# Kernel tuning notes

Measured on AMD Instinct MI355X. Metric: run time of the kernel, lower is better.

Reference implementation:

```python
import jax, jax.numpy as jnp
import numpy as np

D_IN = 512
D = 1024      # new_embed_dim
H = 16        # num_heads
HD = D // H   # head_dim


def setup_inputs() -> dict:
    key = jax.random.key(0)
    ks = jax.random.split(key, 16)
    g = lambda k, shape, fan: jax.random.normal(k, shape, jnp.float32) / np.sqrt(fan)
    return {
        "x1": jax.random.normal(ks[0], (16, 1, D_IN), jnp.float32),
        "x2": jax.random.normal(ks[1], (16, 4096, D_IN), jnp.float32),
        "x3": jax.random.normal(ks[2], (16, 4096, D_IN), jnp.float32),
        # embedding1 (for x1) and embedding2 (used for BOTH x2 and x3, per source)
        "We1": g(ks[3], (D_IN, D), D_IN), "be1": jnp.zeros((D,), jnp.float32),
        "We2": g(ks[4], (D_IN, D), D_IN), "be2": jnp.zeros((D,), jnp.float32),
        "Wq": g(ks[5], (D, D), D), "bq": jnp.zeros((D,), jnp.float32),
        "Wk": g(ks[6], (D, D), D), "bk": jnp.zeros((D,), jnp.float32),
        "Wv": g(ks[7], (D, D), D), "bv": jnp.zeros((D,), jnp.float32),
        "Wo": g(ks[8], (D, D), D), "bo": jnp.zeros((D,), jnp.float32),
    }


def reference(x1, x2, x3, We1, be1, We2, be2, Wq, bq, Wk, bk, Wv, bv, Wo, bo):
    B = x1.shape[0]
    # embeddings (x3 intentionally uses embedding2's weights, matching source)
    x1e = x1 @ We1 + be1                      # [B,1,D]
    x2e = x2 @ We2 + be2                      # [B,S,D]
    x3e = x3 @ We2 + be2                      # [B,S,D]
    q = (x1e @ Wq + bq).reshape(B, -1, H, HD).transpose(0, 2, 1, 3)  # [B,H,1,HD]
    k = (x2e @ Wk + bk).reshape(B, -1, H, HD).transpose(0, 2, 1, 3)  # [B,H,S,HD]
    v = (x3e @ Wv + bv).reshape(B, -1, H, HD).transpose(0, 2, 1, 3)  # [B,H,S,HD]
    scale = jnp.asarray(np.sqrt(HD), q.dtype)
    attn = jax.nn.softmax(jnp.einsum("bhqd,bhkd->bhqk", q, k) / scale, axis=-1)
    # dropout is identity at inference (keras training=False default)
    av = jnp.einsum("bhqk,bhkd->bhqd", attn, v)          # [B,H,1,HD]
    av = av.transpose(0, 2, 1, 3).reshape(B, -1, D)      # [B,1,D]
    out = av @ Wo + bo                                   # [B,1,D]
    return jnp.squeeze(out, axis=1)                      # [B,D]
```

## Files before the change

kernel.cpp:

```cpp
#include <hip/hip_runtime.h>


#define DIN 512
#define DD  1024
#define NH  16
#define HD  64
#define BB  16
#define SS  4096
#define NCH 64

__device__ __forceinline__ int wave_id() {
    return __builtin_amdgcn_readfirstlane((int)(threadIdx.x >> 6));
}

__device__ __forceinline__ void tile_transpose(const float* __restrict__ in,
                                               float* __restrict__ out,
                                               int R, int C, int rblk, int cblk) {
    __shared__ float tl[32][33];
    const int tx = threadIdx.x & 31, ty = threadIdx.x >> 5;
    const int c0 = cblk * 32, r0 = rblk * 32;
#pragma unroll
    for (int k = 0; k < 4; ++k)
        tl[ty + k * 8][tx] = in[(size_t)(r0 + ty + k * 8) * C + c0 + tx];
    __syncthreads();
#pragma unroll
    for (int k = 0; k < 4; ++k)
        out[(size_t)(c0 + ty + k * 8) * R + r0 + tx] = tl[tx][ty + k * 8];
}

__global__ __launch_bounds__(256) void k_prep(const float* __restrict__ We2,
                                              const float* __restrict__ Wk,
                                              const float* __restrict__ be1,
                                              const float* __restrict__ bq,
                                              const float* __restrict__ bv,
                                              const float* __restrict__ bo,
                                              float* __restrict__ We2t,
                                              float* __restrict__ WkT,
                                              float* __restrict__ x1e,
                                              float* __restrict__ qb,
                                              float* __restrict__ av,
                                              float* __restrict__ out) {
    const int bx = blockIdx.x;
    if (bx < 512) {
        tile_transpose(We2, We2t, DIN, DD, bx >> 5, bx & 31);
    } else if (bx < 1536) {
        const int lb = bx - 512;
        tile_transpose(Wk, WkT, DD, DD, lb >> 5, lb & 31);
    } else {
        const int b = bx - 1536;
#pragma unroll
        for (int k = 0; k < 4; ++k) {
            const int c = k * 256 + threadIdx.x;
            x1e[(size_t)b * DD + c] = be1[c];
            qb[(size_t)b * DD + c]  = bq[c];
            av[(size_t)b * DD + c]  = bv[c];
            out[(size_t)b * DD + c] = bo[c];
        }
    }
}

template <int K, int N, int KS, bool HASB>
__global__ __launch_bounds__(256) void k_bmv2(const float* __restrict__ in,
                                              const float* __restrict__ W,
                                              const float* __restrict__ bias,
                                              float* __restrict__ out) {
    const int l = threadIdx.x & 63;
    const int c = blockIdx.x * 64 + l;
    const int wv = wave_id();
    constexpr int KCH = K / KS;
    constexpr int SUB = KCH / 4;
    const float* inb = in + (size_t)blockIdx.y * 16 * K;
    float acc[16];
#pragma unroll
    for (int r = 0; r < 16; ++r) acc[r] = 0.f;
    const int i0 = blockIdx.z * KCH + wv * SUB;
#pragma unroll 4
    for (int i = i0; i < i0 + SUB; ++i) {
        const float wval = W[(size_t)i * N + c];
#pragma unroll
        for (int r = 0; r < 16; ++r) acc[r] += inb[(size_t)r * K + i] * wval;
    }
    __shared__ float red[4][16][64];
#pragma unroll
    for (int r = 0; r < 16; ++r) red[wv][r][l] = acc[r];
    __syncthreads();
#pragma unroll
    for (int k = 0; k < 4; ++k) {
        const int r = wv + k * 4;
        float v = red[0][r][l] + red[1][r][l] + red[2][r][l] + red[3][r][l];
        float* dst = out + ((size_t)blockIdx.y * 16 + r) * N + c;
        if (KS == 1) {
            if (HASB) v += bias[c];
            *dst = v;
        } else {
            atomicAdd(dst, v);
        }
    }
}

__global__ __launch_bounds__(256) void k_u2(const float* __restrict__ q,
                                            const float* __restrict__ WkT,
                                            float* __restrict__ u) {
    const int h = blockIdx.y;
    const int l = threadIdx.x & 63;
    const int c = blockIdx.x * 64 + l;
    const int wv = wave_id();
    float acc[16];
#pragma unroll
    for (int bb = 0; bb < 16; ++bb) acc[bb] = 0.f;
#pragma unroll 4
    for (int dk = 0; dk < 16; ++dk) {
        const int d = wv * 16 + dk;
        const float wval = WkT[(size_t)(h * HD + d) * DD + c];
#pragma unroll
        for (int bb = 0; bb < 16; ++bb)
            acc[bb] += q[(size_t)bb * DD + h * HD + d] * wval;
    }
    __shared__ float red[4][16][64];
#pragma unroll
    for (int bb = 0; bb < 16; ++bb) red[wv][bb][l] = acc[bb];
    __syncthreads();
#pragma unroll
    for (int k = 0; k < 4; ++k) {
        const int bb = wv + k * 4;
        float v = red[0][bb][l] + red[1][bb][l] + red[2][bb][l] + red[3][bb][l];
        u[((size_t)bb * NH + h) * DD + c] = v;
    }
}

__global__ __launch_bounds__(512, 8) void k_attn(const float* __restrict__ x2,
                                                 const float* __restrict__ x3,
                                                 const float* __restrict__ w,
                                                 float* __restrict__ gp,
                                                 float* __restrict__ mls) {
    __shared__ __align__(16) float4 tile[64 * 33];
    __shared__ __align__(16) float etab[64 * 20];

    const int b = blockIdx.y, ch = blockIdx.x;
    const int l = threadIdx.x & 63;
    const int wv = wave_id();
    const int h0 = wv * 2;
    const int s0 = ch * 64;
    const float4* wp = (const float4*)(w + ((size_t)b * NH + h0) * DIN);
    const float4* x2f = (const float4*)x2 + ((size_t)b * SS + s0) * (DIN / 4);

    float a0 = 0.f, a1 = 0.f;
    for (int kt = 0; kt < 4; ++kt) {
#pragma unroll
        for (int k = 0; k < 4; ++k) {
            const int idx = threadIdx.x + k * 512;
            const int row = idx >> 5, c4 = idx & 31;
            tile[row * 33 + c4] = x2f[(size_t)row * 128 + kt * 32 + c4];
        }
        __syncthreads();
#pragma unroll 8
        for (int c4 = 0; c4 < 32; ++c4) {
            const float4 x = tile[l * 33 + c4];
            const float4 q0 = wp[kt * 32 + c4];
            const float4 q1 = wp[128 + kt * 32 + c4];
            a0 += x.x * q0.x + x.y * q0.y + x.z * q0.z + x.w * q0.w;
            a1 += x.x * q1.x + x.y * q1.y + x.z * q1.z + x.w * q1.w;
        }
        __syncthreads();
    }

    const float sc0 = a0 * 0.125f, sc1 = a1 * 0.125f;
    float m0 = sc0, m1 = sc1;
#pragma unroll
    for (int off = 1; off < 64; off <<= 1) {
        m0 = fmaxf(m0, __shfl_xor(m0, off));
        m1 = fmaxf(m1, __shfl_xor(m1, off));
    }
    const float e0 = __expf(sc0 - m0), e1 = __expf(sc1 - m1);
    etab[l * 20 + h0]     = e0;
    etab[l * 20 + h0 + 1] = e1;
    float ls0 = e0, ls1 = e1;
#pragma unroll
    for (int off = 1; off < 64; off <<= 1) {
        ls0 += __shfl_xor(ls0, off);
        ls1 += __shfl_xor(ls1, off);
    }
    if (l == 0) {
        float* dst = mls + (((size_t)b * NCH + ch) * NH + h0) * 2;
        dst[0] = m0; dst[1] = ls0;
        dst[2] = m1; dst[3] = ls1;
    }
    __syncthreads();

    const int col = wv * 64 + l;
    const float* x3c = x3 + ((size_t)b * SS + s0) * DIN + col;
    float acc[16];
#pragma unroll
    for (int h = 0; h < 16; ++h) acc[h] = 0.f;

    float x0 = x3c[0];
    float x1 = x3c[DIN];
    float x2r = x3c[2 * DIN];
    float x3r = x3c[3 * DIN];
#pragma unroll 4
    for (int j = 0; j < 64; ++j) {
        const float xv = x0;
        x0 = x1; x1 = x2r; x2r = x3r;
        const int jn = (j + 4 < 64) ? (j + 4) : 63;
        x3r = x3c[(size_t)jn * DIN];
        const float4 ea = *(const float4*)&etab[j * 20];
        const float4 eb = *(const float4*)&etab[j * 20 + 4];
        const float4 ec = *(const float4*)&etab[j * 20 + 8];
        const float4 ed = *(const float4*)&etab[j * 20 + 12];
        acc[0]  += ea.x * xv;  acc[1]  += ea.y * xv;
        acc[2]  += ea.z * xv;  acc[3]  += ea.w * xv;
        acc[4]  += eb.x * xv;  acc[5]  += eb.y * xv;
        acc[6]  += eb.z * xv;  acc[7]  += eb.w * xv;
        acc[8]  += ec.x * xv;  acc[9]  += ec.y * xv;
        acc[10] += ec.z * xv;  acc[11] += ec.w * xv;
        acc[12] += ed.x * xv;  acc[13] += ed.y * xv;
        acc[14] += ed.z * xv;  acc[15] += ed.w * xv;
    }

    float* gb = gp + ((size_t)(b * NCH + ch) * NH) * DIN + col;
#pragma unroll
    for (int h = 0; h < 16; ++h)
        gb[(size_t)h * DIN] = acc[h];
}

__global__ __launch_bounds__(256) void k_greduce2(const float* __restrict__ gp,
                                                  const float* __restrict__ mls,
                                                  float* __restrict__ g) {
    const int bx = blockIdx.x;
    const int pair = bx >> 1;
    const int b = pair >> 4, h = pair & 15;
    const int i = (bx & 1) * 256 + threadIdx.x;
    const float* mbase = mls + ((size_t)b * NCH * NH + h) * 2;
    float M = -1e30f;
#pragma unroll 8
    for (int ch = 0; ch < NCH; ++ch)
        M = fmaxf(M, mbase[(size_t)ch * NH * 2]);
    float L = 0.f;
#pragma unroll 8
    for (int ch = 0; ch < NCH; ++ch)
        L += __expf(mbase[(size_t)ch * NH * 2] - M) * mbase[(size_t)ch * NH * 2 + 1];
    const float invL = 1.f / L;
    const float* gpb = gp + ((size_t)(b * NCH) * NH + h) * DIN + i;
    float acc = 0.f;
#pragma unroll 8
    for (int ch = 0; ch < NCH; ++ch)
        acc += __expf(mbase[(size_t)ch * NH * 2] - M) * gpb[(size_t)ch * NH * DIN];
    g[(size_t)pair * DIN + i] = acc * invL;
}

__global__ __launch_bounds__(256) void k_av_at(const float* __restrict__ G2,
                                               const float* __restrict__ Wv,
                                               float* __restrict__ av) {
    const int h = blockIdx.x;
    const int l = threadIdx.x & 63;
    const int wv = wave_id();
    const int c0 = blockIdx.y * 128 + wv * 32;
    float acc[16];
#pragma unroll
    for (int bb = 0; bb < 16; ++bb) acc[bb] = 0.f;
#pragma unroll 4
    for (int c = c0; c < c0 + 32; ++c) {
        const float wval = Wv[(size_t)c * DD + h * HD + l];
#pragma unroll
        for (int bb = 0; bb < 16; ++bb)
            acc[bb] += G2[((size_t)bb * NH + h) * DD + c] * wval;
    }
    __shared__ float red[4][16][64];
#pragma unroll
    for (int bb = 0; bb < 16; ++bb) red[wv][bb][l] = acc[bb];
    __syncthreads();
#pragma unroll
    for (int k = 0; k < 4; ++k) {
        const int bb = wv + k * 4;
        float v = red[0][bb][l] + red[1][bb][l] + red[2][bb][l] + red[3][bb][l];
        atomicAdd(&av[(size_t)bb * DD + h * HD + l], v);
    }
}

extern "C" void kernel_launch(void* const* d_in, const int* in_sizes, int n_in,
                              void* d_out, int out_size, void* d_ws, size_t ws_size,
                              hipStream_t stream) {
    const float* x1  = (const float*)d_in[0];
    const float* x2  = (const float*)d_in[1];
    const float* x3  = (const float*)d_in[2];
    const float* We1 = (const float*)d_in[3];
    const float* be1 = (const float*)d_in[4];
    const float* We2 = (const float*)d_in[5];
    const float* be2 = (const float*)d_in[6];
    const float* Wq  = (const float*)d_in[7];
    const float* bq  = (const float*)d_in[8];
    const float* Wk  = (const float*)d_in[9];
    const float* bk  = (const float*)d_in[10];
    const float* Wv  = (const float*)d_in[11];
    const float* bv  = (const float*)d_in[12];
    const float* Wo  = (const float*)d_in[13];
    const float* bo  = (const float*)d_in[14];
    (void)bk;
    float* out = (float*)d_out;

    char* ws = (char*)d_ws;
    size_t off = 0;
    auto alloc = [&](size_t bytes) -> void* {
        void* p = ws + off;
        off = (off + bytes + 255) & ~(size_t)255;
        return p;
    };
    float* We2t = (float*)alloc((size_t)DD * DIN * 4);
    float* WkT  = (float*)alloc((size_t)DD * DD * 4);
    float* x1e  = (float*)alloc((size_t)BB * DD * 4);
    float* qb   = (float*)alloc((size_t)BB * DD * 4);
    float* u    = (float*)alloc((size_t)BB * NH * DD * 4);
    float* wv_  = (float*)alloc((size_t)BB * NH * DIN * 4);
    float* g    = (float*)alloc((size_t)BB * NH * DIN * 4);
    float* G2   = (float*)alloc((size_t)BB * NH * DD * 4);
    float* av   = (float*)alloc((size_t)BB * DD * 4);
    float* gp   = (float*)alloc((size_t)BB * NCH * NH * DIN * 4);
    float* mls  = (float*)alloc((size_t)BB * NCH * NH * 2 * 4);

    k_prep<<<1552, 256, 0, stream>>>(We2, Wk, be1, bq, bv, bo,
                                     We2t, WkT, x1e, qb, av, out);
    k_bmv2<DIN, DD, 8, false><<<dim3(DD / 64, 1, 8), 256, 0, stream>>>(x1, We1, nullptr, x1e);
    k_bmv2<DD, DD, 8, false><<<dim3(DD / 64, 1, 8), 256, 0, stream>>>(x1e, Wq, nullptr, qb);
    k_u2<<<dim3(DD / 64, NH), 256, 0, stream>>>(qb, WkT, u);
    k_bmv2<DD, DIN, 1, false><<<dim3(DIN / 64, BB * NH / 16, 1), 256, 0, stream>>>(u, We2t, nullptr, wv_);
    k_attn<<<dim3(NCH, BB), 512, 0, stream>>>(x2, x3, wv_, gp, mls);
    k_greduce2<<<BB * NH * 2, 256, 0, stream>>>(gp, mls, g);
    k_bmv2<DIN, DD, 1, true><<<dim3(DD / 64, BB * NH / 16, 1), 256, 0, stream>>>(g, We2, be2, G2);
    k_av_at<<<dim3(NH, 8), 256, 0, stream>>>(G2, Wv, av);
    k_bmv2<DD, DD, 8, false><<<dim3(DD / 64, 1, 8), 256, 0, stream>>>(av, Wo, nullptr, out);
}
```

Measured before the change: 446.9 us.

## Prefetch x2 tiles into registers and vectorize x3 weighted-sum loads

The score phase of the attention kernel now loads the next x2 tile into registers while the current tile is being consumed from shared memory. This overlaps global-load latency with compute and drops one barrier per iteration. The value phase is remapped so each wave handles 4 heads across 4 contiguous columns and uses float4 loads and stores for x3 and the partial outputs. This replaces scalar 16-head accumulation, cutting load instruction count and LDS reads at the cost of more live registers.

```diff
diff --git a/kernel.cpp b/kernel.cpp
--- a/kernel.cpp
+++ b/kernel.cpp
@@ -144,15 +144,27 @@
     const float4* wp = (const float4*)(w + ((size_t)b * NH + h0) * DIN);
     const float4* x2f = (const float4*)x2 + ((size_t)b * SS + s0) * (DIN / 4);
 
+    const int srow = threadIdx.x >> 5;
+    const int sc4  = threadIdx.x & 31;
+    float4 r0 = x2f[(size_t)(srow)      * 128 + sc4];
+    float4 r1 = x2f[(size_t)(srow + 16) * 128 + sc4];
+    float4 r2 = x2f[(size_t)(srow + 32) * 128 + sc4];
+    float4 r3 = x2f[(size_t)(srow + 48) * 128 + sc4];
     float a0 = 0.f, a1 = 0.f;
     for (int kt = 0; kt < 4; ++kt) {
-#pragma unroll
-        for (int k = 0; k < 4; ++k) {
-            const int idx = threadIdx.x + k * 512;
-            const int row = idx >> 5, c4 = idx & 31;
-            tile[row * 33 + c4] = x2f[(size_t)row * 128 + kt * 32 + c4];
+        __syncthreads();
+        tile[(srow)      * 33 + sc4] = r0;
+        tile[(srow + 16) * 33 + sc4] = r1;
+        tile[(srow + 32) * 33 + sc4] = r2;
+        tile[(srow + 48) * 33 + sc4] = r3;
+        __syncthreads();
+        if (kt < 3) {
+            const int kc = (kt + 1) * 32 + sc4;
+            r0 = x2f[(size_t)(srow)      * 128 + kc];
+            r1 = x2f[(size_t)(srow + 16) * 128 + kc];
+            r2 = x2f[(size_t)(srow + 32) * 128 + kc];
+            r3 = x2f[(size_t)(srow + 48) * 128 + kc];
         }
-        __syncthreads();
 #pragma unroll 8
         for (int c4 = 0; c4 < 32; ++c4) {
             const float4 x = tile[l * 33 + c4];
@@ -161,7 +173,6 @@
             a0 += x.x * q0.x + x.y * q0.y + x.z * q0.z + x.w * q0.w;
             a1 += x.x * q1.x + x.y * q1.y + x.z * q1.z + x.w * q1.w;
         }
-        __syncthreads();
     }
 
     const float sc0 = a0 * 0.125f, sc1 = a1 * 0.125f;
@@ -187,40 +198,35 @@
     }
     __syncthreads();
 
-    const int col = wv * 64 + l;
-    const float* x3c = x3 + ((size_t)b * SS + s0) * DIN + col;
-    float acc[16];
-#pragma unroll
-    for (int h = 0; h < 16; ++h) acc[h] = 0.f;
-
-    float x0 = x3c[0];
-    float x1 = x3c[DIN];
-    float x2r = x3c[2 * DIN];
-    float x3r = x3c[3 * DIN];
+    const int colh = wv & 1;
+    const int h4 = (wv >> 1) * 4;
+    const float4* x3f = (const float4*)(x3 + ((size_t)b * SS + s0) * DIN)
+                        + colh * 64 + l;
+    float4 A0 = make_float4(0.f, 0.f, 0.f, 0.f);
+    float4 A1 = make_float4(0.f, 0.f, 0.f, 0.f);
+    float4 A2 = make_float4(0.f, 0.f, 0.f, 0.f);
+    float4 A3 = make_float4(0.f, 0.f, 0.f, 0.f);
+
+    float4 p0 = x3f[0 * 128], p1 = x3f[1 * 128];
+    float4 p2 = x3f[2 * 128], p3 = x3f[3 * 128];
 #pragma unroll 4
     for (int j = 0; j < 64; ++j) {
-        const float xv = x0;
-        x0 = x1; x1 = x2r; x2r = x3r;
+        const float4 xv = p0;
+        p0 = p1; p1 = p2; p2 = p3;
         const int jn = (j + 4 < 64) ? (j + 4) : 63;
-        x3r = x3c[(size_t)jn * DIN];
-        const float4 ea = *(const float4*)&etab[j * 20];
-        const float4 eb = *(const float4*)&etab[j * 20 + 4];
-        const float4 ec = *(const float4*)&etab[j * 20 + 8];
-        const float4 ed = *(const float4*)&etab[j * 20 + 12];
-        acc[0]  += ea.x * xv;  acc[1]  += ea.y * xv;
-        acc[2]  += ea.z * xv;  acc[3]  += ea.w * xv;
-        acc[4]  += eb.x * xv;  acc[5]  += eb.y * xv;
-        acc[6]  += eb.z * xv;  acc[7]  += eb.w * xv;
-        acc[8]  += ec.x * xv;  acc[9]  += ec.y * xv;
-        acc[10] += ec.z * xv;  acc[11] += ec.w * xv;
-        acc[12] += ed.x * xv;  acc[13] += ed.y * xv;
-        acc[14] += ed.z * xv;  acc[15] += ed.w * xv;
-    }
-
-    float* gb = gp + ((size_t)(b * NCH + ch) * NH) * DIN + col;
-#pragma unroll
-    for (int h = 0; h < 16; ++h)
-        gb[(size_t)h * DIN] = acc[h];
+        p3 = x3f[(size_t)jn * 128];
+        const float4 e4 = *(const float4*)&etab[j * 20 + h4];
+        A0.x += e4.x * xv.x; A0.y += e4.x * xv.y; A0.z += e4.x * xv.z; A0.w += e4.x * xv.w;
+        A1.x += e4.y * xv.x; A1.y += e4.y * xv.y; A1.z += e4.y * xv.z; A1.w += e4.y * xv.w;
+        A2.x += e4.z * xv.x; A2.y += e4.z * xv.y; A2.z += e4.z * xv.z; A2.w += e4.z * xv.w;
+        A3.x += e4.w * xv.x; A3.y += e4.w * xv.y; A3.z += e4.w * xv.z; A3.w += e4.w * xv.w;
+    }
+
+    float* gb = gp + ((size_t)(b * NCH + ch) * NH + h4) * DIN + colh * 256 + 4 * l;
+    *(float4*)(gb + 0 * DIN) = A0;
+    *(float4*)(gb + 1 * DIN) = A1;
+    *(float4*)(gb + 2 * DIN) = A2;
+    *(float4*)(gb + 3 * DIN) = A3;
 }
 
 __global__ __launch_bounds__(256) void k_greduce2(const float* __restrict__ gp,
```

Result: no change. 446.0 us (-0.2%).
